# Kernel tuning notes

Measured on AMD Instinct MI355X. Metric: run time of the kernel, lower is better.

## Reference

```python
import jax, jax.numpy as jnp
import numpy as np


def setup_inputs() -> dict:
    key = jax.random.key(0)
    ks = jax.random.split(key, 18)
    B, T, L, C = 16, 512, 50, 7
    H = 512
    s = 0.05
    inp = {
        "phone_data": jax.random.normal(ks[0], (B, T, L, C), jnp.float32),
        "h0": jax.random.normal(ks[1], (B, H), jnp.float32),
        "conv1_w": jax.random.normal(ks[2], (128, 7, 11), jnp.float32) * s,
        "conv1_b": jax.random.normal(ks[3], (128,), jnp.float32) * s,
        "conv2_w": jax.random.normal(ks[4], (256, 128, 9), jnp.float32) * s,
        "conv2_b": jax.random.normal(ks[5], (256,), jnp.float32) * s,
        "fc1_w": jax.random.normal(ks[6], (1024, 1536), jnp.float32) * s,
        "fc1_b": jax.random.normal(ks[7], (1024,), jnp.float32) * s,
        "fc2_w": jax.random.normal(ks[8], (512, 1024), jnp.float32) * s,
        "fc2_b": jax.random.normal(ks[9], (512,), jnp.float32) * s,
        "gru_wih": jax.random.normal(ks[10], (3 * H, H), jnp.float32) * s,
        "gru_whh": jax.random.normal(ks[11], (3 * H, H), jnp.float32) * s,
        "gru_bih": jax.random.normal(ks[12], (3 * H,), jnp.float32) * s,
        "gru_bhh": jax.random.normal(ks[13], (3 * H,), jnp.float32) * s,
        "fc3_w": jax.random.normal(ks[14], (1, H), jnp.float32) * s,
        "fc3_b": jax.random.normal(ks[15], (1,), jnp.float32) * s,
    }
    return inp


def reference(phone_data, h0, conv1_w, conv1_b, conv2_w, conv2_b,
              fc1_w, fc1_b, fc2_w, fc2_b,
              gru_wih, gru_whh, gru_bih, gru_bhh, fc3_w, fc3_b):
    B, T, L, C = phone_data.shape
    N = B * T
    # ---- batched CNN + FC feature extractor (independent per frame) ----
    x = phone_data.reshape(N, L, C).transpose(0, 2, 1)  # [N, 7, 50]
    y = jax.lax.conv_general_dilated(
        x, conv1_w, (1,), 'VALID',
        dimension_numbers=('NCH', 'OIH', 'NCH')) + conv1_b[None, :, None]  # [N,128,40]
    y = y.reshape(N, 128, 20, 2).max(-1)  # maxpool k=2,s=2 -> [N,128,20]
    y = jax.lax.conv_general_dilated(
        y, conv2_w, (1,), 'VALID',
        dimension_numbers=('NCH', 'OIH', 'NCH')) + conv2_b[None, :, None]  # [N,256,12]
    y = y.reshape(N, 256, 6, 2).max(-1)  # [N,256,6]
    feat = y.reshape(N, 1536)            # Flatten(0): channel-major, matches torch
    feat = feat @ fc1_w.T + fc1_b        # [N,1024]
    feat = feat @ fc2_w.T + fc2_b        # [N,512]
    feat = feat.reshape(B, T, 512)

    # ---- sequential GRUCell recurrence (PyTorch GRUCell math) ----
    def cell(h, x_t):
        gi = x_t @ gru_wih.T + gru_bih   # [B, 3H]
        gh = h @ gru_whh.T + gru_bhh     # [B, 3H]
        ir, iz, in_ = jnp.split(gi, 3, axis=-1)
        hr, hz, hn = jnp.split(gh, 3, axis=-1)
        r = jax.nn.sigmoid(ir + hr)
        z = jax.nn.sigmoid(iz + hz)
        n = jnp.tanh(in_ + r * hn)
        h_new = (1 - z) * n + z * h
        # original code calls hx.detach() every step
        h_new = jax.lax.stop_gradient(h_new)
        return h_new, h_new

    _, hs = jax.lax.scan(cell, h0, feat.transpose(1, 0, 2))  # hs: [T,B,512]
    out = hs @ fc3_w.T + fc3_b  # [T,B,1]
    return out.transpose(1, 0, 2)  # [B,T,1]
```

## Files before the change

kernel.cpp:

```cpp
#include <hip/hip_runtime.h>
#include <hip/hip_bf16.h>
#include <math.h>
#include <stdint.h>

typedef __attribute__((ext_vector_type(8))) short short8;
typedef __attribute__((ext_vector_type(4))) float f32x4;
typedef __attribute__((ext_vector_type(4))) unsigned int uint4v;

#define T_ 512

__device__ __forceinline__ unsigned short bf16rn(float f) {
  union { float f; unsigned u; } x; x.f = f;
  unsigned r = x.u + 0x7FFF + ((x.u >> 16) & 1);
  return (unsigned short)(r >> 16);
}

__device__ __forceinline__ void gload16(const void* gsrc, void* ldst) {
  __builtin_amdgcn_global_load_lds(
      (const __attribute__((address_space(1))) unsigned int*)gsrc,
      (__attribute__((address_space(3))) unsigned int*)ldst, 16, 0, 0);
}

__device__ __forceinline__ void wg_barrier() {
  __builtin_amdgcn_sched_barrier(0);
  asm volatile("s_waitcnt lgkmcnt(0)" ::: "memory");
  __builtin_amdgcn_sched_barrier(0);
  __builtin_amdgcn_s_barrier();
  __builtin_amdgcn_sched_barrier(0);
}

__global__ __launch_bounds__(256) void conv1_kernel(
    const float* __restrict__ phone, const float* __restrict__ w1,
    const float* __restrict__ b1, ushort* __restrict__ out1b) {
  __shared__ float ws[128 * 77];
  __shared__ float bs[128];
  __shared__ float xs[8][7][52];
  const int tid = threadIdx.x;
  const int n0 = blockIdx.x * 8;
  for (int idx = tid; idx < 9856; idx += 256) ws[idx] = w1[idx];
  if (tid < 128) bs[tid] = b1[tid];
  for (int idx = tid; idx < 2800; idx += 256) {
    int fi = idx / 350, r = idx - fi * 350;
    int ll = r / 7, c = r - ll * 7;
    xs[fi][c][ll] = phone[(size_t)(n0 + fi) * 350 + r];
  }
  __syncthreads();

  const int o = tid >> 1, ph = tid & 1;
  const float* wo = ws + o * 77;
  const float bb = bs[o];
  for (int fi = 0; fi < 8; ++fi) {
    float acc0[10], acc1[10];
#pragma unroll
    for (int q = 0; q < 10; ++q) { acc0[q] = 0.f; acc1[q] = 0.f; }
    for (int i = 0; i < 7; ++i) {
      float wr[11];
#pragma unroll
      for (int k = 0; k < 11; ++k) wr[k] = wo[i * 11 + k];
#pragma unroll
      for (int q = 0; q < 10; ++q) {
        int p = ph * 10 + q;
        int base = 2 * p;
        float xv[12];
#pragma unroll
        for (int j = 0; j < 12; ++j) xv[j] = xs[fi][i][base + j];
        float s0 = 0.f, s1 = 0.f;
#pragma unroll
        for (int k = 0; k < 11; ++k) {
          s0 += xv[k] * wr[k];
          s1 += xv[k + 1] * wr[k];
        }
        acc0[q] += s0;
        acc1[q] += s1;
      }
    }
#pragma unroll
    for (int q = 0; q < 10; ++q) {
      int p = ph * 10 + q;
      out1b[((size_t)(n0 + fi) * 128 + o) * 20 + p] =
          bf16rn(fmaxf(acc0[q], acc1[q]) + bb);
    }
  }
}

__global__ __launch_bounds__(256) void f32_to_bf16(
    const float* __restrict__ src, ushort* __restrict__ dst, int n4) {
  int i = blockIdx.x * 256 + threadIdx.x;
  if (i < n4) {
    float4 v = ((const float4*)src)[i];
    ushort4 o;
    o.x = bf16rn(v.x); o.y = bf16rn(v.y); o.z = bf16rn(v.z); o.w = bf16rn(v.w);
    ((ushort4*)dst)[i] = o;
  }
}

__global__ __launch_bounds__(256) void stage_h0(
    const float* __restrict__ h0, unsigned long long* __restrict__ hxt) {
  const int tid = threadIdx.x;
#pragma unroll
  for (int k = 0; k < 16; ++k) {
    int idx = tid + k * 256;
    int g = idx >> 11, rem = idx & 2047;
    int s = rem >> 7, w_i = rem & 127;
    int b8 = (w_i >> 2) & 7, fqk = w_i >> 5, p2 = w_i & 3;
    int b = g * 8 + b8;
    int d = s * 32 + fqk * 8 + p2 * 2;
    float2 h2 = *(const float2*)(h0 + (size_t)b * 512 + d);
    unsigned pk = (unsigned)bf16rn(h2.x) | ((unsigned)bf16rn(h2.y) << 16);
    hxt[(size_t)g * 4096 + s * 128 + w_i] = (unsigned long long)pk;
  }
}

template <int AM, int EM>
__global__ __launch_bounds__(256) void gemm_bf16(
    const ushort* __restrict__ A, const ushort* __restrict__ W,
    const float* __restrict__ bias, void* __restrict__ Cout,
    int K, int lda, int ldc) {
  __shared__ ushort As[128 * 64];
  __shared__ ushort Bs[128 * 64];
  __shared__ ushort tbl[1152];
  const int tid = threadIdx.x;
  const int l = tid & 63, wv = tid >> 6;
  const int wr = wv >> 1, wc = wv & 1;
  const int fr = l & 15, fq = l >> 4;
  const int bm0 = blockIdx.x * 128, bn0 = blockIdx.y * 128;

  if (AM == 1) {
    for (int idx = tid; idx < 1152; idx += 256) {
      int i2 = idx / 9, kp = idx - i2 * 9;
      tbl[idx] = (ushort)(i2 * 20 + kp);
    }
    __syncthreads();
  }

  f32x4 acc[4][4];
#pragma unroll
  for (int mi = 0; mi < 4; ++mi)
#pragma unroll
    for (int ni = 0; ni < 4; ++ni) acc[mi][ni] = (f32x4)0.f;

  const int pr8 = l >> 3;
  const int pc = l & 7;
  const int nkt = K >> 6;
  for (int kt = 0; kt < nkt; ++kt) {
    const int k0 = kt << 6;
#pragma unroll
    for (int i = 0; i < 4; ++i) {
      int q = wv * 4 + i;
      int prow = q * 8 + pr8;
      int lc = pc ^ (prow & 7);
      gload16(W + (size_t)(bn0 + prow) * K + k0 + lc * 8, &Bs[q * 512]);
    }
    if (AM == 0) {
#pragma unroll
      for (int i = 0; i < 4; ++i) {
        int q = wv * 4 + i;
        int prow = q * 8 + pr8;
        int lc = pc ^ (prow & 7);
        gload16(A + (size_t)(bm0 + prow) * lda + k0 + lc * 8, &As[q * 512]);
      }
    } else {
#pragma unroll
      for (int q = 0; q < 16; ++q) {
        int idx = tid + q * 256;
        int row = idx >> 5, c0 = (idx & 31) * 2;
        int m = bm0 + row;
        int n = m / 12, pos = m - n * 12;
        int kk = k0 + c0;
        const ushort* an = A + (size_t)n * 2560 + pos;
        uint e0 = an[tbl[kk]];
        uint e1 = an[tbl[kk + 1]];
        *(uint*)&As[row * 64 + (((c0 >> 3) ^ (row & 7)) << 3) + (c0 & 7)] =
            e0 | (e1 << 16);
      }
    }
    __syncthreads();
#pragma unroll
    for (int ks = 0; ks < 2; ++ks) {
      short8 af[4], bfr[4];
#pragma unroll
      for (int mi = 0; mi < 4; ++mi) {
        int row = wr * 64 + mi * 16 + fr;
        af[mi] = *(const short8*)&As[row * 64 + (((ks * 4 + fq) ^ (row & 7)) << 3)];
      }
#pragma unroll
      for (int ni = 0; ni < 4; ++ni) {
        int row = wc * 64 + ni * 16 + fr;
        bfr[ni] = *(const short8*)&Bs[row * 64 + (((ks * 4 + fq) ^ (row & 7)) << 3)];
      }
#pragma unroll
      for (int mi = 0; mi < 4; ++mi)
#pragma unroll
        for (int ni = 0; ni < 4; ++ni)
          acc[mi][ni] = __builtin_amdgcn_mfma_f32_16x16x32_bf16(
              af[mi], bfr[ni], acc[mi][ni], 0, 0, 0);
    }
    __syncthreads();
  }

#pragma unroll
  for (int ni = 0; ni < 4; ++ni) {
    int col = bn0 + wc * 64 + ni * 16 + fr;
    float bv = bias[col];
#pragma unroll
    for (int mi = 0; mi < 4; ++mi) {
      int mbase = bm0 + wr * 64 + mi * 16 + fq * 4;
      if (EM == 0) {
        ushort* C = (ushort*)Cout;
#pragma unroll
        for (int j = 0; j < 4; ++j)
          C[(size_t)(mbase + j) * ldc + col] = bf16rn(acc[mi][ni][j] + bv);
      } else if (EM == 1) {
        ushort* C = (ushort*)Cout;
#pragma unroll
        for (int j = 0; j < 4; j += 2) {
          int m = mbase + j;
          int n = m / 12, pos = m - n * 12;
          float v = fmaxf(acc[mi][ni][j], acc[mi][ni][j + 1]) + bv;
          C[(size_t)n * 1536 + col * 6 + (pos >> 1)] = bf16rn(v);
        }
      } else {
        float* C = (float*)Cout;
#pragma unroll
        for (int j = 0; j < 4; ++j) {
          int m = mbase + j;
          int b = m >> 9, tt = m & 511;
          C[((size_t)tt * 16 + b) * 1536 + col] = acc[mi][ni][j] + bv;
        }
      }
    }
  }
}

__global__ __launch_bounds__(384) void gru_persistent(
    const float* __restrict__ h0, const float* __restrict__ gi,
    const float* __restrict__ whh, const float* __restrict__ bhh,
    float* __restrict__ hsbuf, unsigned long long* __restrict__ hxt) {
  __shared__ float gh_lds[12 * 256];
  __shared__ unsigned afl[16 * 64 * 4];
  const int tid = threadIdx.x;
  const int g = blockIdx.x >> 3, wp = blockIdx.x & 7;
  const int l = tid & 63, v = tid >> 6;
  const int fr = l & 15, fq = l >> 4;
  unsigned long long* hxg = hxt + (size_t)g * 4096;

  const int t0 = 2 * v, t1 = 2 * v + 1;
  const int o0 = (t0 >> 2) * 512 + wp * 64 + (t0 & 3) * 16 + fr;
  const int o1 = (t1 >> 2) * 512 + wp * 64 + (t1 & 3) * 16 + fr;
  short8 bf0[16], bf1[16];
#pragma unroll
  for (int s = 0; s < 16; ++s) {
    const float* wp0 = whh + (size_t)o0 * 512 + s * 32 + fq * 8;
    const float* wp1 = whh + (size_t)o1 * 512 + s * 32 + fq * 8;
    float4 a0 = *(const float4*)wp0, a1 = *(const float4*)(wp0 + 4);
    float4 c0 = *(const float4*)wp1, c1 = *(const float4*)(wp1 + 4);
    short8 x, y;
    x[0] = (short)bf16rn(a0.x); x[1] = (short)bf16rn(a0.y);
    x[2] = (short)bf16rn(a0.z); x[3] = (short)bf16rn(a0.w);
    x[4] = (short)bf16rn(a1.x); x[5] = (short)bf16rn(a1.y);
    x[6] = (short)bf16rn(a1.z); x[7] = (short)bf16rn(a1.w);
    y[0] = (short)bf16rn(c0.x); y[1] = (short)bf16rn(c0.y);
    y[2] = (short)bf16rn(c0.z); y[3] = (short)bf16rn(c0.w);
    y[4] = (short)bf16rn(c1.x); y[5] = (short)bf16rn(c1.y);
    y[6] = (short)bf16rn(c1.z); y[7] = (short)bf16rn(c1.w);
    bf0[s] = x; bf1[s] = y;
  }
  const float bo0 = bhh[o0], bo1 = bhh[o1];

  const int b8 = tid >> 5, jp = tid & 31, jl = jp * 2;
  const bool gthr = (tid < 256);
  const int pt = tid - 256;
  const int bglob = g * 8 + b8;
  const int jglob = wp * 64 + jl;
  float hA = 0.f, hB = 0.f;
  float giC0 = 0.f, giC1 = 0.f, giC2 = 0.f, giC3 = 0.f, giC4 = 0.f, giC5 = 0.f;
  float giN0 = 0.f, giN1 = 0.f, giN2 = 0.f, giN3 = 0.f, giN4 = 0.f, giN5 = 0.f;
  if (gthr) {
    float2 h2 = *(const float2*)(h0 + (size_t)bglob * 512 + jglob);
    hA = h2.x; hB = h2.y;
    const float* g0 = gi + (size_t)bglob * 1536 + jglob;
    float2 r0 = *(const float2*)(g0);
    float2 r1 = *(const float2*)(g0 + 512);
    float2 r2 = *(const float2*)(g0 + 1024);
    giC0 = r0.x; giC3 = r0.y; giC1 = r1.x; giC4 = r1.y; giC2 = r2.x; giC5 = r2.y;
    const float* g1 = gi + (size_t)(16 + bglob) * 1536 + jglob;
    float2 s0 = *(const float2*)(g1);
    float2 s1 = *(const float2*)(g1 + 512);
    float2 s2 = *(const float2*)(g1 + 1024);
    giN0 = s0.x; giN3 = s0.y; giN1 = s1.x; giN4 = s1.y; giN2 = s2.x; giN5 = s2.y;
  }

  if (!gthr) {
    const int ps = pt >> 3;
    const int pw0 = (pt & 7) * 2;
    const unsigned long long* base = hxg + ps * 128;
    uint4v r[8];
    for (;;) {
#pragma unroll
      for (int q = 0; q < 8; ++q)
        asm volatile("global_load_dwordx4 %0, %1, off sc0 sc1"
                     : "=v"(r[q]) : "v"(base + pw0 + q * 16));
      asm volatile("s_waitcnt vmcnt(0)" ::: "memory");
      __builtin_amdgcn_sched_barrier(0);
      bool ok = true;
#pragma unroll
      for (int q = 0; q < 8; ++q)
        ok = ok & (r[q].y == 0u) & (r[q].w == 0u);
      if (ok) break;
    }
#pragma unroll
    for (int q = 0; q < 8; ++q) {
      int w_i = pw0 + q * 16;
      int lane = ((w_i >> 2) & 7) + 16 * (w_i >> 5);
      *(uint2*)&afl[(ps * 64 + lane) * 4 + (w_i & 3)] = make_uint2(r[q].x, r[q].z);
    }
  }
  wg_barrier();

  for (int t = 0; t < T_; ++t) {
    f32x4 e0 = (f32x4)0.f, q0 = (f32x4)0.f, e1 = (f32x4)0.f, q1 = (f32x4)0.f;
#pragma unroll
    for (int s = 0; s < 16; s += 2) {
      union { uint4v u; short8 s8; } ca, cb;
      ca.u = *(const uint4v*)&afl[((s + 0) * 64 + l) * 4];
      cb.u = *(const uint4v*)&afl[((s + 1) * 64 + l) * 4];
      e0 = __builtin_amdgcn_mfma_f32_16x16x32_bf16(ca.s8, bf0[s], e0, 0, 0, 0);
      q0 = __builtin_amdgcn_mfma_f32_16x16x32_bf16(cb.s8, bf0[s + 1], q0, 0, 0, 0);
      e1 = __builtin_amdgcn_mfma_f32_16x16x32_bf16(ca.s8, bf1[s], e1, 0, 0, 0);
      q1 = __builtin_amdgcn_mfma_f32_16x16x32_bf16(cb.s8, bf1[s + 1], q1, 0, 0, 0);
    }
#pragma unroll
    for (int j = 0; j < 4; ++j) {
      gh_lds[t0 * 256 + (fq * 4 + j) * 16 + fr] = e0[j] + q0[j] + bo0;
      gh_lds[t1 * 256 + (fq * 4 + j) * 16 + fr] = e1[j] + q1[j] + bo1;
    }
    wg_barrier();

    if (gthr) {
      const int hh = jl >> 4, c = jl & 15;
      float2 rr = *(const float2*)&gh_lds[(0 + hh) * 256 + b8 * 16 + c];
      float2 zz = *(const float2*)&gh_lds[(4 + hh) * 256 + b8 * 16 + c];
      float2 nn = *(const float2*)&gh_lds[(8 + hh) * 256 + b8 * 16 + c];
      float rgA = __builtin_amdgcn_rcpf(1.f + __expf(-(giC0 + rr.x)));
      float rgB = __builtin_amdgcn_rcpf(1.f + __expf(-(giC3 + rr.y)));
      float zgA = __builtin_amdgcn_rcpf(1.f + __expf(-(giC1 + zz.x)));
      float zgB = __builtin_amdgcn_rcpf(1.f + __expf(-(giC4 + zz.y)));
      float eA = __expf(2.f * (giC2 + rgA * nn.x));
      float eB = __expf(2.f * (giC5 + rgB * nn.y));
      float ngA = 1.f - 2.f * __builtin_amdgcn_rcpf(eA + 1.f);
      float ngB = 1.f - 2.f * __builtin_amdgcn_rcpf(eB + 1.f);
      hA = (1.f - zgA) * ngA + zgA * hA;
      hB = (1.f - zgB) * ngB + zgB * hB;
      if (t + 1 < T_) {
        unsigned pk = (unsigned)bf16rn(hA) | ((unsigned)bf16rn(hB) << 16);
        unsigned long long payload =
            (unsigned long long)pk | ((unsigned long long)(unsigned)(t + 1) << 32);
        int s = wp * 2 + (jl >> 5);
        int w_i = (((jl & 31) >> 3) * 8 + b8) * 4 + (jp & 3);
        __hip_atomic_store(hxg + ((t + 1) & 1) * 2048 + s * 128 + w_i, payload,
                           __ATOMIC_RELAXED, __HIP_MEMORY_SCOPE_AGENT);
      }
      *(float2*)(hsbuf + ((size_t)t * 16 + bglob) * 512 + jglob) =
          make_float2(hA, hB);
      giC0 = giN0; giC1 = giN1; giC2 = giN2;
      giC3 = giN3; giC4 = giN4; giC5 = giN5;
      if (t + 2 < T_) {
        const float* gb = gi + ((size_t)(t + 2) * 16 + bglob) * 1536 + jglob;
        float2 r0 = *(const float2*)(gb);
        float2 r1 = *(const float2*)(gb + 512);
        float2 r2 = *(const float2*)(gb + 1024);
        giN0 = r0.x; giN3 = r0.y; giN1 = r1.x; giN4 = r1.y; giN2 = r2.x; giN5 = r2.y;
      }
    } else if (t + 1 < T_) {
      const int ps = pt >> 3;
      const int pw0 = (pt & 7) * 2;
      const unsigned long long* base =
          hxg + ((t + 1) & 1) * 2048 + ps * 128;
      const unsigned tag = (unsigned)(t + 1);
      uint4v r[8];
      for (;;) {
#pragma unroll
        for (int q = 0; q < 8; ++q)
          asm volatile("global_load_dwordx4 %0, %1, off sc0 sc1"
                       : "=v"(r[q]) : "v"(base + pw0 + q * 16));
        asm volatile("s_waitcnt vmcnt(0)" ::: "memory");
        __builtin_amdgcn_sched_barrier(0);
        bool ok = true;
#pragma unroll
        for (int q = 0; q < 8; ++q)
          ok = ok & (r[q].y == tag) & (r[q].w == tag);
        if (ok) break;
      }
#pragma unroll
      for (int q = 0; q < 8; ++q) {
        int w_i = pw0 + q * 16;
        int lane = ((w_i >> 2) & 7) + 16 * (w_i >> 5);
        *(uint2*)&afl[(ps * 64 + lane) * 4 + (w_i & 3)] = make_uint2(r[q].x, r[q].z);
      }
    }
    wg_barrier();
  }
}

__global__ __launch_bounds__(256) void fc3_kernel(
    const float* __restrict__ hs, const float* __restrict__ w3,
    const float* __restrict__ b3, float* __restrict__ out) {
  __shared__ float w[512];
  const int tid = threadIdx.x;
  w[tid] = w3[tid];
  w[tid + 256] = w3[tid + 256];
  __syncthreads();
  const int gidx = blockIdx.x * 256 + tid;
  const int b = gidx >> 9, t = gidx & 511;
  const float4* hr = (const float4*)(hs + ((size_t)t * 16 + b) * 512);
  const float4* wr = (const float4*)w;
  float acc = 0.f;
#pragma unroll 8
  for (int kc = 0; kc < 128; ++kc) {
    float4 h = hr[kc], ww = wr[kc];
    acc += h.x * ww.x + h.y * ww.y + h.z * ww.z + h.w * ww.w;
  }
  out[gidx] = acc + b3[0];
}

extern "C" void kernel_launch(void* const* d_in, const int* in_sizes, int n_in,
                              void* d_out, int out_size, void* d_ws,
                              size_t ws_size, hipStream_t stream) {
  const float* phone = (const float*)d_in[0];
  const float* h0    = (const float*)d_in[1];
  const float* w1    = (const float*)d_in[2];
  const float* b1    = (const float*)d_in[3];
  const float* w2    = (const float*)d_in[4];
  const float* b2    = (const float*)d_in[5];
  const float* fc1w  = (const float*)d_in[6];
  const float* fc1b  = (const float*)d_in[7];
  const float* fc2w  = (const float*)d_in[8];
  const float* fc2b  = (const float*)d_in[9];
  const float* wih   = (const float*)d_in[10];
  const float* whh   = (const float*)d_in[11];
  const float* bih   = (const float*)d_in[12];
  const float* bhh   = (const float*)d_in[13];
  const float* w3    = (const float*)d_in[14];
  const float* b3    = (const float*)d_in[15];
  float* out = (float*)d_out;

  char* ws = (char*)d_ws;
  ushort* out1b = (ushort*)(ws + 0);
  ushort* feat2 = (ushort*)(ws + 41943040);
  ushort* feat3 = (ushort*)(ws + 67108864);
  ushort* feat4 = (ushort*)(ws + 83886080);
  float*  gibuf = (float*) (ws + 92274688);
  float*  hsbuf = (float*) (ws + 142606336);
  ushort* w2b   = (ushort*)(ws + 159383552);
  ushort* fc1wb = (ushort*)(ws + 159973376);
  ushort* fc2wb = (ushort*)(ws + 163119104);
  ushort* wihb  = (ushort*)(ws + 164167680);
  unsigned long long* hxt = (unsigned long long*)(ws + 67108864);

  f32_to_bf16<<<288, 256, 0, stream>>>(w2, w2b, 73728);
  f32_to_bf16<<<1536, 256, 0, stream>>>(fc1w, fc1wb, 393216);
  f32_to_bf16<<<512, 256, 0, stream>>>(fc2w, fc2wb, 131072);
  f32_to_bf16<<<768, 256, 0, stream>>>(wih, wihb, 196608);

  conv1_kernel<<<1024, 256, 0, stream>>>(phone, w1, b1, out1b);
  gemm_bf16<1, 1><<<dim3(768, 2), 256, 0, stream>>>(out1b, w2b, b2, feat2, 1152, 0, 0);
  gemm_bf16<0, 0><<<dim3(64, 8), 256, 0, stream>>>(feat2, fc1wb, fc1b, feat3, 1536, 1536, 1024);
  gemm_bf16<0, 0><<<dim3(64, 4), 256, 0, stream>>>(feat3, fc2wb, fc2b, feat4, 1024, 1024, 512);
  gemm_bf16<0, 2><<<dim3(64, 12), 256, 0, stream>>>(feat4, wihb, bih, gibuf, 512, 512, 1536);

  hipMemsetAsync(hxt, 0, 65536, stream);
  stage_h0<<<1, 256, 0, stream>>>(h0, hxt);
  gru_persistent<<<16, 384, 0, stream>>>(h0, gibuf, whh, bhh, hsbuf, hxt);

  fc3_kernel<<<32, 256, 0, stream>>>(hsbuf, w3, b3, out);
}
```

Baseline: 1.495 ms.

## Repartition persistent GRU into 4-batch groups with wider column slices per block

The persistent GRU kernel is reorganized so each of 16 blocks handles 4 batch rows and 128 hidden columns instead of 8 rows and 64 columns. Each block now runs 8 waves of 3 MFMA tiles each. The exchange buffer is halved, and each poller thread loads fewer 16-byte words per step. Separately, the four weight-conversion launches are merged into one kernel to cut launch overhead. The aim is to shrink per-step synchronization traffic across blocks. In exchange, each block computes more gate outputs per step, and half of every MFMA tile's rows are padding, which raises the serial critical path.

```diff
diff --git a/kernel.cpp b/kernel.cpp
--- a/kernel.cpp
+++ b/kernel.cpp
@@ -83,15 +83,23 @@
   }
 }
 
-__global__ __launch_bounds__(256) void f32_to_bf16(
-    const float* __restrict__ src, ushort* __restrict__ dst, int n4) {
+__global__ __launch_bounds__(256) void f32_to_bf16_multi(
+    const float* __restrict__ s0, ushort* __restrict__ d0,
+    const float* __restrict__ s1, ushort* __restrict__ d1,
+    const float* __restrict__ s2, ushort* __restrict__ d2,
+    const float* __restrict__ s3, ushort* __restrict__ d3) {
+  const int n0 = 73728, n1 = 393216, n2 = 131072, n3 = 196608;
   int i = blockIdx.x * 256 + threadIdx.x;
-  if (i < n4) {
-    float4 v = ((const float4*)src)[i];
-    ushort4 o;
-    o.x = bf16rn(v.x); o.y = bf16rn(v.y); o.z = bf16rn(v.z); o.w = bf16rn(v.w);
-    ((ushort4*)dst)[i] = o;
-  }
+  const float* s; ushort* d; int off;
+  if (i < n0) { s = s0; d = d0; off = i; }
+  else if (i < n0 + n1) { s = s1; d = d1; off = i - n0; }
+  else if (i < n0 + n1 + n2) { s = s2; d = d2; off = i - n0 - n1; }
+  else if (i < n0 + n1 + n2 + n3) { s = s3; d = d3; off = i - n0 - n1 - n2; }
+  else return;
+  float4 v = ((const float4*)s)[off];
+  ushort4 o;
+  o.x = bf16rn(v.x); o.y = bf16rn(v.y); o.z = bf16rn(v.z); o.w = bf16rn(v.w);
+  ((ushort4*)d)[off] = o;
 }
 
 __global__ __launch_bounds__(256) void stage_h0(
@@ -100,14 +108,14 @@
 #pragma unroll
   for (int k = 0; k < 16; ++k) {
     int idx = tid + k * 256;
-    int g = idx >> 11, rem = idx & 2047;
-    int s = rem >> 7, w_i = rem & 127;
-    int b8 = (w_i >> 2) & 7, fqk = w_i >> 5, p2 = w_i & 3;
-    int b = g * 8 + b8;
-    int d = s * 32 + fqk * 8 + p2 * 2;
-    float2 h2 = *(const float2*)(h0 + (size_t)b * 512 + d);
+    int g = idx >> 10, rem = idx & 1023;
+    int s = rem >> 6, w = rem & 63;
+    int b4 = (w >> 2) & 3, fqk = w >> 4, p2 = w & 3;
+    int b = g * 4 + b4;
+    int D = s * 32 + fqk * 8 + p2 * 2;
+    float2 h2 = *(const float2*)(h0 + (size_t)b * 512 + D);
     unsigned pk = (unsigned)bf16rn(h2.x) | ((unsigned)bf16rn(h2.y) << 16);
-    hxt[(size_t)g * 4096 + s * 128 + w_i] = (unsigned long long)pk;
+    hxt[(size_t)g * 2048 + rem] = (unsigned long long)pk;
   }
 }
 
@@ -232,46 +240,56 @@
   }
 }
 
-__global__ __launch_bounds__(384) void gru_persistent(
+__global__ __launch_bounds__(512) void gru_persistent(
     const float* __restrict__ h0, const float* __restrict__ gi,
     const float* __restrict__ whh, const float* __restrict__ bhh,
     float* __restrict__ hsbuf, unsigned long long* __restrict__ hxt) {
-  __shared__ float gh_lds[12 * 256];
+  __shared__ float gh_lds[24 * 64];
   __shared__ unsigned afl[16 * 64 * 4];
   const int tid = threadIdx.x;
-  const int g = blockIdx.x >> 3, wp = blockIdx.x & 7;
+  const int g = blockIdx.x >> 2, wp = blockIdx.x & 3;
   const int l = tid & 63, v = tid >> 6;
   const int fr = l & 15, fq = l >> 4;
-  unsigned long long* hxg = hxt + (size_t)g * 4096;
-
-  const int t0 = 2 * v, t1 = 2 * v + 1;
-  const int o0 = (t0 >> 2) * 512 + wp * 64 + (t0 & 3) * 16 + fr;
-  const int o1 = (t1 >> 2) * 512 + wp * 64 + (t1 & 3) * 16 + fr;
-  short8 bf0[16], bf1[16];
+  unsigned long long* hxg = hxt + (size_t)g * 2048;
+
+  for (int i = tid; i < 4096; i += 512) afl[i] = 0u;
+
+  const int tA = 3 * v, tB = 3 * v + 1, tC = 3 * v + 2;
+  const int oA = (tA >> 3) * 512 + wp * 128 + (tA & 7) * 16 + fr;
+  const int oB = (tB >> 3) * 512 + wp * 128 + (tB & 7) * 16 + fr;
+  const int oC = (tC >> 3) * 512 + wp * 128 + (tC & 7) * 16 + fr;
+  short8 bfA[16], bfB[16], bfC[16];
 #pragma unroll
   for (int s = 0; s < 16; ++s) {
-    const float* wp0 = whh + (size_t)o0 * 512 + s * 32 + fq * 8;
-    const float* wp1 = whh + (size_t)o1 * 512 + s * 32 + fq * 8;
-    float4 a0 = *(const float4*)wp0, a1 = *(const float4*)(wp0 + 4);
-    float4 c0 = *(const float4*)wp1, c1 = *(const float4*)(wp1 + 4);
-    short8 x, y;
+    const float* pA = whh + (size_t)oA * 512 + s * 32 + fq * 8;
+    const float* pB = whh + (size_t)oB * 512 + s * 32 + fq * 8;
+    const float* pC = whh + (size_t)oC * 512 + s * 32 + fq * 8;
+    float4 a0 = *(const float4*)pA, a1 = *(const float4*)(pA + 4);
+    float4 b0 = *(const float4*)pB, b1 = *(const float4*)(pB + 4);
+    float4 c0 = *(const float4*)pC, c1 = *(const float4*)(pC + 4);
+    short8 x, y, z;
     x[0] = (short)bf16rn(a0.x); x[1] = (short)bf16rn(a0.y);
     x[2] = (short)bf16rn(a0.z); x[3] = (short)bf16rn(a0.w);
     x[4] = (short)bf16rn(a1.x); x[5] = (short)bf16rn(a1.y);
     x[6] = (short)bf16rn(a1.z); x[7] = (short)bf16rn(a1.w);
-    y[0] = (short)bf16rn(c0.x); y[1] = (short)bf16rn(c0.y);
-    y[2] = (short)bf16rn(c0.z); y[3] = (short)bf16rn(c0.w);
-    y[4] = (short)bf16rn(c1.x); y[5] = (short)bf16rn(c1.y);
-    y[6] = (short)bf16rn(c1.z); y[7] = (short)bf16rn(c1.w);
-    bf0[s] = x; bf1[s] = y;
-  }
-  const float bo0 = bhh[o0], bo1 = bhh[o1];
-
-  const int b8 = tid >> 5, jp = tid & 31, jl = jp * 2;
+    y[0] = (short)bf16rn(b0.x); y[1] = (short)bf16rn(b0.y);
+    y[2] = (short)bf16rn(b0.z); y[3] = (short)bf16rn(b0.w);
+    y[4] = (short)bf16rn(b1.x); y[5] = (short)bf16rn(b1.y);
+    y[6] = (short)bf16rn(b1.z); y[7] = (short)bf16rn(b1.w);
+    z[0] = (short)bf16rn(c0.x); z[1] = (short)bf16rn(c0.y);
+    z[2] = (short)bf16rn(c0.z); z[3] = (short)bf16rn(c0.w);
+    z[4] = (short)bf16rn(c1.x); z[5] = (short)bf16rn(c1.y);
+    z[6] = (short)bf16rn(c1.z); z[7] = (short)bf16rn(c1.w);
+    bfA[s] = x; bfB[s] = y; bfC[s] = z;
+  }
+  const float boA = bhh[oA], boB = bhh[oB], boC = bhh[oC];
+
+  const int b4 = tid >> 6, jp = tid & 63, jl = jp * 2;
   const bool gthr = (tid < 256);
+  const bool pthr = (tid >= 256 && tid < 384);
   const int pt = tid - 256;
-  const int bglob = g * 8 + b8;
-  const int jglob = wp * 64 + jl;
+  const int bglob = g * 4 + (b4 & 3);
+  const int jglob = wp * 128 + jl;
   float hA = 0.f, hB = 0.f;
   float giC0 = 0.f, giC1 = 0.f, giC2 = 0.f, giC3 = 0.f, giC4 = 0.f, giC5 = 0.f;
   float giN0 = 0.f, giN1 = 0.f, giN2 = 0.f, giN3 = 0.f, giN4 = 0.f, giN5 = 0.f;
@@ -289,58 +307,60 @@
     float2 s2 = *(const float2*)(g1 + 1024);
     giN0 = s0.x; giN3 = s0.y; giN1 = s1.x; giN4 = s1.y; giN2 = s2.x; giN5 = s2.y;
   }
-
-  if (!gthr) {
+  __syncthreads();
+
+  if (pthr) {
     const int ps = pt >> 3;
-    const int pw0 = (pt & 7) * 2;
-    const unsigned long long* base = hxg + ps * 128;
-    uint4v r[8];
+    const int w0 = (pt & 7) * 8;
+    const unsigned long long* base = hxg + ps * 64 + w0;
+    uint4v r[4];
     for (;;) {
 #pragma unroll
-      for (int q = 0; q < 8; ++q)
+      for (int q = 0; q < 4; ++q)
         asm volatile("global_load_dwordx4 %0, %1, off sc0 sc1"
-                     : "=v"(r[q]) : "v"(base + pw0 + q * 16));
+                     : "=v"(r[q]) : "v"(base + q * 2));
       asm volatile("s_waitcnt vmcnt(0)" ::: "memory");
       __builtin_amdgcn_sched_barrier(0);
       bool ok = true;
 #pragma unroll
-      for (int q = 0; q < 8; ++q)
+      for (int q = 0; q < 4; ++q)
         ok = ok & (r[q].y == 0u) & (r[q].w == 0u);
       if (ok) break;
     }
 #pragma unroll
-    for (int q = 0; q < 8; ++q) {
-      int w_i = pw0 + q * 16;
-      int lane = ((w_i >> 2) & 7) + 16 * (w_i >> 5);
-      *(uint2*)&afl[(ps * 64 + lane) * 4 + (w_i & 3)] = make_uint2(r[q].x, r[q].z);
+    for (int q = 0; q < 4; ++q) {
+      int w = w0 + 2 * q;
+      int lane = ((w >> 2) & 3) | ((w >> 4) << 4);
+      *(uint2*)&afl[(ps * 64 + lane) * 4 + (w & 3)] = make_uint2(r[q].x, r[q].z);
     }
   }
   wg_barrier();
 
   for (int t = 0; t < T_; ++t) {
-    f32x4 e0 = (f32x4)0.f, q0 = (f32x4)0.f, e1 = (f32x4)0.f, q1 = (f32x4)0.f;
-#pragma unroll
-    for (int s = 0; s < 16; s += 2) {
-      union { uint4v u; short8 s8; } ca, cb;
-      ca.u = *(const uint4v*)&afl[((s + 0) * 64 + l) * 4];
-      cb.u = *(const uint4v*)&afl[((s + 1) * 64 + l) * 4];
-      e0 = __builtin_amdgcn_mfma_f32_16x16x32_bf16(ca.s8, bf0[s], e0, 0, 0, 0);
-      q0 = __builtin_amdgcn_mfma_f32_16x16x32_bf16(cb.s8, bf0[s + 1], q0, 0, 0, 0);
-      e1 = __builtin_amdgcn_mfma_f32_16x16x32_bf16(ca.s8, bf1[s], e1, 0, 0, 0);
-      q1 = __builtin_amdgcn_mfma_f32_16x16x32_bf16(cb.s8, bf1[s + 1], q1, 0, 0, 0);
-    }
-#pragma unroll
-    for (int j = 0; j < 4; ++j) {
-      gh_lds[t0 * 256 + (fq * 4 + j) * 16 + fr] = e0[j] + q0[j] + bo0;
-      gh_lds[t1 * 256 + (fq * 4 + j) * 16 + fr] = e1[j] + q1[j] + bo1;
+    f32x4 aA = (f32x4)0.f, aB = (f32x4)0.f, aC = (f32x4)0.f;
+#pragma unroll
+    for (int s = 0; s < 16; ++s) {
+      union { uint4v u; short8 s8; } ca;
+      ca.u = *(const uint4v*)&afl[(s * 64 + l) * 4];
+      aA = __builtin_amdgcn_mfma_f32_16x16x32_bf16(ca.s8, bfA[s], aA, 0, 0, 0);
+      aB = __builtin_amdgcn_mfma_f32_16x16x32_bf16(ca.s8, bfB[s], aB, 0, 0, 0);
+      aC = __builtin_amdgcn_mfma_f32_16x16x32_bf16(ca.s8, bfC[s], aC, 0, 0, 0);
+    }
+    if (fq == 0) {
+#pragma unroll
+      for (int j = 0; j < 4; ++j) {
+        gh_lds[tA * 64 + j * 16 + fr] = aA[j] + boA;
+        gh_lds[tB * 64 + j * 16 + fr] = aB[j] + boB;
+        gh_lds[tC * 64 + j * 16 + fr] = aC[j] + boC;
+      }
     }
     wg_barrier();
 
     if (gthr) {
-      const int hh = jl >> 4, c = jl & 15;
-      float2 rr = *(const float2*)&gh_lds[(0 + hh) * 256 + b8 * 16 + c];
-      float2 zz = *(const float2*)&gh_lds[(4 + hh) * 256 + b8 * 16 + c];
-      float2 nn = *(const float2*)&gh_lds[(8 + hh) * 256 + b8 * 16 + c];
+      const int tl = jl >> 4, c = jl & 15;
+      float2 rr = *(const float2*)&gh_lds[(0 + tl) * 64 + b4 * 16 + c];
+      float2 zz = *(const float2*)&gh_lds[(8 + tl) * 64 + b4 * 16 + c];
+      float2 nn = *(const float2*)&gh_lds[(16 + tl) * 64 + b4 * 16 + c];
       float rgA = __builtin_amdgcn_rcpf(1.f + __expf(-(giC0 + rr.x)));
       float rgB = __builtin_amdgcn_rcpf(1.f + __expf(-(giC3 + rr.y)));
       float zgA = __builtin_amdgcn_rcpf(1.f + __expf(-(giC1 + zz.x)));
@@ -355,9 +375,9 @@
         unsigned pk = (unsigned)bf16rn(hA) | ((unsigned)bf16rn(hB) << 16);
         unsigned long long payload =
             (unsigned long long)pk | ((unsigned long long)(unsigned)(t + 1) << 32);
-        int s = wp * 2 + (jl >> 5);
-        int w_i = (((jl & 31) >> 3) * 8 + b8) * 4 + (jp & 3);
-        __hip_atomic_store(hxg + ((t + 1) & 1) * 2048 + s * 128 + w_i, payload,
+        int s = wp * 4 + (jl >> 5);
+        int w_i = (((jl >> 3) & 3) * 4 + b4) * 4 + ((jl & 7) >> 1);
+        __hip_atomic_store(hxg + ((t + 1) & 1) * 1024 + s * 64 + w_i, payload,
                            __ATOMIC_RELAXED, __HIP_MEMORY_SCOPE_AGENT);
       }
       *(float2*)(hsbuf + ((size_t)t * 16 + bglob) * 512 + jglob) =
@@ -371,31 +391,31 @@
         float2 r2 = *(const float2*)(gb + 1024);
         giN0 = r0.x; giN3 = r0.y; giN1 = r1.x; giN4 = r1.y; giN2 = r2.x; giN5 = r2.y;
       }
-    } else if (t + 1 < T_) {
+    } else if (pthr && t + 1 < T_) {
       const int ps = pt >> 3;
-      const int pw0 = (pt & 7) * 2;
+      const int w0 = (pt & 7) * 8;
       const unsigned long long* base =
-          hxg + ((t + 1) & 1) * 2048 + ps * 128;
+          hxg + ((t + 1) & 1) * 1024 + ps * 64 + w0;
       const unsigned tag = (unsigned)(t + 1);
-      uint4v r[8];
+      uint4v r[4];
       for (;;) {
 #pragma unroll
-        for (int q = 0; q < 8; ++q)
+        for (int q = 0; q < 4; ++q)
           asm volatile("global_load_dwordx4 %0, %1, off sc0 sc1"
-                       : "=v"(r[q]) : "v"(base + pw0 + q * 16));
+                       : "=v"(r[q]) : "v"(base + q * 2));
         asm volatile("s_waitcnt vmcnt(0)" ::: "memory");
         __builtin_amdgcn_sched_barrier(0);
         bool ok = true;
 #pragma unroll
-        for (int q = 0; q < 8; ++q)
+        for (int q = 0; q < 4; ++q)
           ok = ok & (r[q].y == tag) & (r[q].w == tag);
         if (ok) break;
       }
 #pragma unroll
-      for (int q = 0; q < 8; ++q) {
-        int w_i = pw0 + q * 16;
-        int lane = ((w_i >> 2) & 7) + 16 * (w_i >> 5);
-        *(uint2*)&afl[(ps * 64 + lane) * 4 + (w_i & 3)] = make_uint2(r[q].x, r[q].z);
+      for (int q = 0; q < 4; ++q) {
+        int w = w0 + 2 * q;
+        int lane = ((w >> 2) & 3) | ((w >> 4) << 4);
+        *(uint2*)&afl[(ps * 64 + lane) * 4 + (w & 3)] = make_uint2(r[q].x, r[q].z);
       }
     }
     wg_barrier();
@@ -457,10 +477,8 @@
   ushort* wihb  = (ushort*)(ws + 164167680);
   unsigned long long* hxt = (unsigned long long*)(ws + 67108864);
 
-  f32_to_bf16<<<288, 256, 0, stream>>>(w2, w2b, 73728);
-  f32_to_bf16<<<1536, 256, 0, stream>>>(fc1w, fc1wb, 393216);
-  f32_to_bf16<<<512, 256, 0, stream>>>(fc2w, fc2wb, 131072);
-  f32_to_bf16<<<768, 256, 0, stream>>>(wih, wihb, 196608);
+  f32_to_bf16_multi<<<3104, 256, 0, stream>>>(w2, w2b, fc1w, fc1wb,
+                                              fc2w, fc2wb, wih, wihb);
 
   conv1_kernel<<<1024, 256, 0, stream>>>(phone, w1, b1, out1b);
   gemm_bf16<1, 1><<<dim3(768, 2), 256, 0, stream>>>(out1b, w2b, b2, feat2, 1152, 0, 0);
@@ -470,7 +488,7 @@
 
   hipMemsetAsync(hxt, 0, 65536, stream);
   stage_h0<<<1, 256, 0, stream>>>(h0, hxt);
-  gru_persistent<<<16, 384, 0, stream>>>(h0, gibuf, whh, bhh, hsbuf, hxt);
+  gru_persistent<<<16, 512, 0, stream>>>(h0, gibuf, whh, bhh, hsbuf, hxt);
 
   fc3_kernel<<<32, 256, 0, stream>>>(hsbuf, w3, b3, out);
 }
```

Result: slower. 1.529 ms (+2.2%).

## Poll XCD-local hidden-state copy in GRU recurrence, fall back to coherent mirror

Applied to the files above, without the earlier changes.

The GRU kernel now launches 64 blocks but keeps only those whose block index modulo 8 is 0 or 1. The apparent intent is to place each batch group's cooperating blocks on the same XCD. Each producer writes its hidden-state chunk twice: a volatile store to a local copy, and an agent-scope atomic store to a mirror. Consumers first poll the local copy with cheaper sc0-only loads and switch to the sc1 mirror if the tag does not show up within a bounded number of tries. The four weight-conversion launches are also merged into one kernel. The design relies on the assumption that round-robin block placement puts same-group blocks on one XCD sharing an L2, and it adds redundant stores and fallback logic.

```diff
diff --git a/kernel.cpp b/kernel.cpp
--- a/kernel.cpp
+++ b/kernel.cpp
@@ -83,15 +83,23 @@
   }
 }
 
-__global__ __launch_bounds__(256) void f32_to_bf16(
-    const float* __restrict__ src, ushort* __restrict__ dst, int n4) {
+__global__ __launch_bounds__(256) void f32_to_bf16_multi(
+    const float* __restrict__ s0, ushort* __restrict__ d0,
+    const float* __restrict__ s1, ushort* __restrict__ d1,
+    const float* __restrict__ s2, ushort* __restrict__ d2,
+    const float* __restrict__ s3, ushort* __restrict__ d3) {
+  const int n0 = 73728, n1 = 393216, n2 = 131072, n3 = 196608;
   int i = blockIdx.x * 256 + threadIdx.x;
-  if (i < n4) {
-    float4 v = ((const float4*)src)[i];
-    ushort4 o;
-    o.x = bf16rn(v.x); o.y = bf16rn(v.y); o.z = bf16rn(v.z); o.w = bf16rn(v.w);
-    ((ushort4*)dst)[i] = o;
-  }
+  const float* s; ushort* d; int off;
+  if (i < n0) { s = s0; d = d0; off = i; }
+  else if (i < n0 + n1) { s = s1; d = d1; off = i - n0; }
+  else if (i < n0 + n1 + n2) { s = s2; d = d2; off = i - n0 - n1; }
+  else if (i < n0 + n1 + n2 + n3) { s = s3; d = d3; off = i - n0 - n1 - n2; }
+  else return;
+  float4 v = ((const float4*)s)[off];
+  ushort4 o;
+  o.x = bf16rn(v.x); o.y = bf16rn(v.y); o.z = bf16rn(v.z); o.w = bf16rn(v.w);
+  ((ushort4*)d)[off] = o;
 }
 
 __global__ __launch_bounds__(256) void stage_h0(
@@ -104,10 +112,10 @@
     int s = rem >> 7, w_i = rem & 127;
     int b8 = (w_i >> 2) & 7, fqk = w_i >> 5, p2 = w_i & 3;
     int b = g * 8 + b8;
-    int d = s * 32 + fqk * 8 + p2 * 2;
-    float2 h2 = *(const float2*)(h0 + (size_t)b * 512 + d);
+    int D = s * 32 + fqk * 8 + p2 * 2;
+    float2 h2 = *(const float2*)(h0 + (size_t)b * 512 + D);
     unsigned pk = (unsigned)bf16rn(h2.x) | ((unsigned)bf16rn(h2.y) << 16);
-    hxt[(size_t)g * 4096 + s * 128 + w_i] = (unsigned long long)pk;
+    hxt[8192 + (size_t)g * 4096 + s * 128 + w_i] = (unsigned long long)pk;
   }
 }
 
@@ -239,10 +247,24 @@
   __shared__ float gh_lds[12 * 256];
   __shared__ unsigned afl[16 * 64 * 4];
   const int tid = threadIdx.x;
-  const int g = blockIdx.x >> 3, wp = blockIdx.x & 7;
+  const int g = blockIdx.x & 7, wp = blockIdx.x >> 3;
+  if (g >= 2) return;
   const int l = tid & 63, v = tid >> 6;
   const int fr = l & 15, fq = l >> 4;
-  unsigned long long* hxg = hxt + (size_t)g * 4096;
+  unsigned long long* hxl = hxt + (size_t)g * 4096;
+  unsigned long long* hxm = hxt + 8192 + (size_t)g * 4096;
+
+  const int b8 = tid >> 5, jp = tid & 31, jl = jp * 2;
+  const bool gthr = (tid < 256);
+  const int pt = tid - 256;
+
+  int s_w = 0, w_w = 0;
+  if (gthr) {
+    s_w = wp * 2 + (jl >> 5);
+    w_w = (((jl & 31) >> 3) * 8 + b8) * 4 + (jp & 3);
+    *(volatile unsigned long long*)(hxl + s_w * 128 + w_w) = 0ull;
+    *(volatile unsigned long long*)(hxl + 2048 + s_w * 128 + w_w) = 0ull;
+  }
 
   const int t0 = 2 * v, t1 = 2 * v + 1;
   const int o0 = (t0 >> 2) * 512 + wp * 64 + (t0 & 3) * 16 + fr;
@@ -267,9 +289,6 @@
   }
   const float bo0 = bhh[o0], bo1 = bhh[o1];
 
-  const int b8 = tid >> 5, jp = tid & 31, jl = jp * 2;
-  const bool gthr = (tid < 256);
-  const int pt = tid - 256;
   const int bglob = g * 8 + b8;
   const int jglob = wp * 64 + jl;
   float hA = 0.f, hB = 0.f;
@@ -290,29 +309,30 @@
     giN0 = s0.x; giN3 = s0.y; giN1 = s1.x; giN4 = s1.y; giN2 = s2.x; giN5 = s2.y;
   }
 
+  bool useMir = false;
   if (!gthr) {
     const int ps = pt >> 3;
     const int pw0 = (pt & 7) * 2;
-    const unsigned long long* base = hxg + ps * 128;
+    const unsigned long long* base = hxm + ps * 128;
     uint4v r[8];
     for (;;) {
 #pragma unroll
-      for (int q = 0; q < 8; ++q)
+      for (int m = 0; m < 8; ++m)
         asm volatile("global_load_dwordx4 %0, %1, off sc0 sc1"
-                     : "=v"(r[q]) : "v"(base + pw0 + q * 16));
+                     : "=v"(r[m]) : "v"(base + pw0 + m * 16));
       asm volatile("s_waitcnt vmcnt(0)" ::: "memory");
       __builtin_amdgcn_sched_barrier(0);
       bool ok = true;
 #pragma unroll
-      for (int q = 0; q < 8; ++q)
-        ok = ok & (r[q].y == 0u) & (r[q].w == 0u);
+      for (int m = 0; m < 8; ++m)
+        ok = ok & (r[m].y == 0u) & (r[m].w == 0u);
       if (ok) break;
     }
 #pragma unroll
-    for (int q = 0; q < 8; ++q) {
-      int w_i = pw0 + q * 16;
+    for (int m = 0; m < 8; ++m) {
+      int w_i = pw0 + m * 16;
       int lane = ((w_i >> 2) & 7) + 16 * (w_i >> 5);
-      *(uint2*)&afl[(ps * 64 + lane) * 4 + (w_i & 3)] = make_uint2(r[q].x, r[q].z);
+      *(uint2*)&afl[(ps * 64 + lane) * 4 + (w_i & 3)] = make_uint2(r[m].x, r[m].z);
     }
   }
   wg_barrier();
@@ -355,10 +375,10 @@
         unsigned pk = (unsigned)bf16rn(hA) | ((unsigned)bf16rn(hB) << 16);
         unsigned long long payload =
             (unsigned long long)pk | ((unsigned long long)(unsigned)(t + 1) << 32);
-        int s = wp * 2 + (jl >> 5);
-        int w_i = (((jl & 31) >> 3) * 8 + b8) * 4 + (jp & 3);
-        __hip_atomic_store(hxg + ((t + 1) & 1) * 2048 + s * 128 + w_i, payload,
-                           __ATOMIC_RELAXED, __HIP_MEMORY_SCOPE_AGENT);
+        const size_t woff = (size_t)((t + 1) & 1) * 2048 + s_w * 128 + w_w;
+        *(volatile unsigned long long*)(hxl + woff) = payload;
+        __hip_atomic_store(hxm + woff, payload, __ATOMIC_RELAXED,
+                           __HIP_MEMORY_SCOPE_AGENT);
       }
       *(float2*)(hsbuf + ((size_t)t * 16 + bglob) * 512 + jglob) =
           make_float2(hA, hB);
@@ -374,28 +394,49 @@
     } else if (t + 1 < T_) {
       const int ps = pt >> 3;
       const int pw0 = (pt & 7) * 2;
-      const unsigned long long* base =
-          hxg + ((t + 1) & 1) * 2048 + ps * 128;
       const unsigned tag = (unsigned)(t + 1);
+      const size_t poff = (size_t)((t + 1) & 1) * 2048 + ps * 128;
       uint4v r[8];
-      for (;;) {
-#pragma unroll
-        for (int q = 0; q < 8; ++q)
-          asm volatile("global_load_dwordx4 %0, %1, off sc0 sc1"
-                       : "=v"(r[q]) : "v"(base + pw0 + q * 16));
-        asm volatile("s_waitcnt vmcnt(0)" ::: "memory");
-        __builtin_amdgcn_sched_barrier(0);
-        bool ok = true;
-#pragma unroll
-        for (int q = 0; q < 8; ++q)
-          ok = ok & (r[q].y == tag) & (r[q].w == tag);
-        if (ok) break;
-      }
-#pragma unroll
-      for (int q = 0; q < 8; ++q) {
-        int w_i = pw0 + q * 16;
+      bool done = false;
+      if (!useMir && t + 1 >= 9) {
+        const unsigned long long* base = hxl + poff;
+        int iters = 24;
+        do {
+#pragma unroll
+          for (int m = 0; m < 8; ++m)
+            asm volatile("global_load_dwordx4 %0, %1, off sc0"
+                         : "=v"(r[m]) : "v"(base + pw0 + m * 16));
+          asm volatile("s_waitcnt vmcnt(0)" ::: "memory");
+          __builtin_amdgcn_sched_barrier(0);
+          bool ok = true;
+#pragma unroll
+          for (int m = 0; m < 8; ++m)
+            ok = ok & (r[m].y == tag) & (r[m].w == tag);
+          done = ok;
+        } while (!done && --iters);
+        if (!done) useMir = true;
+      }
+      if (!done) {
+        const unsigned long long* base = hxm + poff;
+        for (;;) {
+#pragma unroll
+          for (int m = 0; m < 8; ++m)
+            asm volatile("global_load_dwordx4 %0, %1, off sc0 sc1"
+                         : "=v"(r[m]) : "v"(base + pw0 + m * 16));
+          asm volatile("s_waitcnt vmcnt(0)" ::: "memory");
+          __builtin_amdgcn_sched_barrier(0);
+          bool ok = true;
+#pragma unroll
+          for (int m = 0; m < 8; ++m)
+            ok = ok & (r[m].y == tag) & (r[m].w == tag);
+          if (ok) break;
+        }
+      }
+#pragma unroll
+      for (int m = 0; m < 8; ++m) {
+        int w_i = pw0 + m * 16;
         int lane = ((w_i >> 2) & 7) + 16 * (w_i >> 5);
-        *(uint2*)&afl[(ps * 64 + lane) * 4 + (w_i & 3)] = make_uint2(r[q].x, r[q].z);
+        *(uint2*)&afl[(ps * 64 + lane) * 4 + (w_i & 3)] = make_uint2(r[m].x, r[m].z);
       }
     }
     wg_barrier();
@@ -457,10 +498,8 @@
   ushort* wihb  = (ushort*)(ws + 164167680);
   unsigned long long* hxt = (unsigned long long*)(ws + 67108864);
 
-  f32_to_bf16<<<288, 256, 0, stream>>>(w2, w2b, 73728);
-  f32_to_bf16<<<1536, 256, 0, stream>>>(fc1w, fc1wb, 393216);
-  f32_to_bf16<<<512, 256, 0, stream>>>(fc2w, fc2wb, 131072);
-  f32_to_bf16<<<768, 256, 0, stream>>>(wih, wihb, 196608);
+  f32_to_bf16_multi<<<3104, 256, 0, stream>>>(w2, w2b, fc1w, fc1wb,
+                                              fc2w, fc2wb, wih, wihb);
 
   conv1_kernel<<<1024, 256, 0, stream>>>(phone, w1, b1, out1b);
   gemm_bf16<1, 1><<<dim3(768, 2), 256, 0, stream>>>(out1b, w2b, b2, feat2, 1152, 0, 0);
@@ -468,9 +507,9 @@
   gemm_bf16<0, 0><<<dim3(64, 4), 256, 0, stream>>>(feat3, fc2wb, fc2b, feat4, 1024, 1024, 512);
   gemm_bf16<0, 2><<<dim3(64, 12), 256, 0, stream>>>(feat4, wihb, bih, gibuf, 512, 512, 1536);
 
-  hipMemsetAsync(hxt, 0, 65536, stream);
+  hipMemsetAsync(hxt, 0, 131072, stream);
   stage_h0<<<1, 256, 0, stream>>>(h0, hxt);
-  gru_persistent<<<16, 384, 0, stream>>>(h0, gibuf, whh, bhh, hsbuf, hxt);
+  gru_persistent<<<64, 384, 0, stream>>>(h0, gibuf, whh, bhh, hsbuf, hxt);
 
   fc3_kernel<<<32, 256, 0, stream>>>(hsbuf, w3, b3, out);
 }
```

Result: slower. 1.820 ms (+21.7%).
